# Kernel tuning notes

Measured on AMD Instinct MI355X. Metric: run time of the kernel, lower is better.

Reference implementation:

```python
import jax, jax.numpy as jnp
import numpy as np

B, S, D, H = 2, 2048, 2048, 16
HD = D // H  # head dim = 128

def setup_inputs() -> dict:
    key = jax.random.key(0)
    ks = jax.random.split(key, 5)
    x = jax.random.normal(ks[0], (B, S, D), dtype=jnp.float32)
    # causal mask: True means block that position (per docstring)
    mask = jnp.triu(jnp.ones((S, S), dtype=bool), k=1)
    scale = 1.0 / np.sqrt(D)
    Wq = jax.random.normal(ks[1], (D, D), dtype=jnp.float32) * scale
    Wk = jax.random.normal(ks[2], (D, D), dtype=jnp.float32) * scale
    Wv = jax.random.normal(ks[3], (D, D), dtype=jnp.float32) * scale
    Wo = jax.random.normal(ks[4], (D, D), dtype=jnp.float32) * scale
    return {"x": x, "mask": mask, "Wq": Wq, "Wk": Wk, "Wv": Wv, "Wo": Wo}

def _split_heads(t):
    b, s, _ = t.shape
    return t.reshape(b, s, H, HD).transpose(0, 2, 1, 3)  # (b, h, s, hd)

def reference(x, mask, Wq, Wk, Wv, Wo):
    # nn.Linear(bias=False): y = x @ W.T
    q = _split_heads(x @ Wq.T)
    k = _split_heads(x @ Wk.T)
    v = _split_heads(x @ Wv.T)
    scale = HD ** -0.5
    scores = jnp.einsum('bhqd,bhkd->bhqk', q, k) * scale  # (b,h,s,s)
    scores = jnp.where(mask[None, None, :, :], -jnp.inf, scores)
    weights = jax.nn.softmax(scores, axis=-1)  # dropout is identity at eval
    out = jnp.einsum('bhqk,bhkd->bhqd', weights, v)
    out = out.transpose(0, 2, 1, 3).reshape(x.shape[0], x.shape[1], D)
    return out @ Wo.T
```

## Files before the change

### kernel.cpp

```cpp
#include <hip/hip_runtime.h>
#include <hip/hip_bf16.h>

typedef __bf16 bf16x8 __attribute__((ext_vector_type(8)));
typedef float f32x4 __attribute__((ext_vector_type(4)));
typedef unsigned short ushort8v __attribute__((ext_vector_type(8)));

__device__ __forceinline__ unsigned short f2bf(float f) {
    unsigned int u = __float_as_uint(f);
    u = (u + 0x7fffu + ((u >> 16) & 1u)) >> 16;
    return (unsigned short)u;
}

__device__ __forceinline__ f32x4 mfma16(bf16x8 a, bf16x8 b, f32x4 c) {
    return __builtin_amdgcn_mfma_f32_16x16x32_bf16(a, b, c, 0, 0, 0);
}

__device__ __forceinline__ void store_c(unsigned short* p, float v) { *p = f2bf(v); }
__device__ __forceinline__ void store_c(float* p, float v) { *p = v; }

__global__ __launch_bounds__(256) void cast_f32_bf16(const float* __restrict__ in,
                                                     unsigned short* __restrict__ out,
                                                     int n4) {
    int i = blockIdx.x * blockDim.x + threadIdx.x;
    if (i < n4) {
        float4 f = ((const float4*)in)[i];
        ushort4 u;
        u.x = f2bf(f.x); u.y = f2bf(f.y); u.z = f2bf(f.z); u.w = f2bf(f.w);
        ((ushort4*)out)[i] = u;
    }
}

__global__ __launch_bounds__(256) void transpose_v(const unsigned short* __restrict__ v,
                                                   unsigned short* __restrict__ vt) {
    __shared__ unsigned short t[64][65];
    const int tid = threadIdx.x;
    const int s0 = blockIdx.x * 64;
    const int d0 = blockIdx.y * 64;
    const int bh = blockIdx.z;
    const int b = bh >> 4, h = bh & 15;

#pragma unroll
    for (int i = 0; i < 2; ++i) {
        int idx = i * 256 + tid;
        int r = idx >> 3, c8 = (idx & 7) * 8;
        ushort8v d = *(const ushort8v*)(v + ((size_t)(b * 2048 + s0 + r)) * 2048 + h * 128 + d0 + c8);
#pragma unroll
        for (int j = 0; j < 8; ++j) t[r][c8 + j] = d[j];
    }
    __syncthreads();
#pragma unroll
    for (int i = 0; i < 2; ++i) {
        int idx = i * 256 + tid;
        int dr = idx >> 3, sc8 = (idx & 7) * 8;
        ushort8v o;
#pragma unroll
        for (int j = 0; j < 8; ++j) o[j] = t[sc8 + j][dr];
        *(ushort8v*)(vt + ((size_t)(bh * 128 + d0 + dr)) * 2048 + s0 + sc8) = o;
    }
}

template <typename OUT_T>
__global__ __launch_bounds__(256) void gemm_bt(const unsigned short* __restrict__ A,
                                               const unsigned short* __restrict__ B,
                                               OUT_T* __restrict__ C,
                                               int M, int N, int K) {
    __shared__ __align__(16) unsigned short lA[128 * 64];
    __shared__ __align__(16) unsigned short lB[128 * 64];

    const int tid = threadIdx.x;
    const int w = tid >> 6, lane = tid & 63;
    const int wm = w >> 1, wn = w & 1;
    const int lane16 = lane & 15, g = lane >> 4;
    const int row0 = blockIdx.y * 128, col0 = blockIdx.x * 128;

    f32x4 acc[4][4] = {};

    for (int kt = 0; kt < K; kt += 64) {
#pragma unroll
        for (int i = 0; i < 4; ++i) {
            int ci = (w * 4 + i) * 64 + lane;
            int grow = ci >> 3;
            int gcolb = (ci & 7) * 16;
            size_t aoff = ((size_t)(row0 + grow) * K + kt) * 2 + gcolb;
            size_t boff = ((size_t)(col0 + grow) * K + kt) * 2 + gcolb;
            __builtin_amdgcn_global_load_lds(
                (__attribute__((address_space(1))) void*)(void*)((const char*)A + aoff),
                (__attribute__((address_space(3))) void*)((char*)lA + (w * 4 + i) * 1024),
                16, 0, 0);
            __builtin_amdgcn_global_load_lds(
                (__attribute__((address_space(1))) void*)(void*)((const char*)B + boff),
                (__attribute__((address_space(3))) void*)((char*)lB + (w * 4 + i) * 1024),
                16, 0, 0);
        }
        __syncthreads();
#pragma unroll
        for (int kk = 0; kk < 2; ++kk) {
            bf16x8 aF[4], bF[4];
#pragma unroll
            for (int f = 0; f < 4; ++f) {
                aF[f] = *(const bf16x8*)&lA[(wm * 64 + f * 16 + lane16) * 64 + kk * 32 + g * 8];
                bF[f] = *(const bf16x8*)&lB[(wn * 64 + f * 16 + lane16) * 64 + kk * 32 + g * 8];
            }
#pragma unroll
            for (int fm = 0; fm < 4; ++fm)
#pragma unroll
                for (int fn = 0; fn < 4; ++fn)
                    acc[fm][fn] = mfma16(aF[fm], bF[fn], acc[fm][fn]);
        }
        __syncthreads();
    }

#pragma unroll
    for (int fm = 0; fm < 4; ++fm) {
        int r0 = row0 + wm * 64 + fm * 16 + g * 4;
#pragma unroll
        for (int fn = 0; fn < 4; ++fn) {
            int c = col0 + wn * 64 + fn * 16 + lane16;
#pragma unroll
            for (int r = 0; r < 4; ++r)
                store_c(&C[(size_t)(r0 + r) * N + c], acc[fm][fn][r]);
        }
    }
}

__global__ __launch_bounds__(256) void attn_causal(const unsigned short* __restrict__ Q,
                                                   const unsigned short* __restrict__ K,
                                                   const unsigned short* __restrict__ VT,
                                                   unsigned short* __restrict__ O) {
    __shared__ __align__(16) unsigned short lK[64 * 128];
    __shared__ __align__(16) unsigned short lVt[128 * 64];
    __shared__ __align__(16) unsigned short lP[4][16 * 80];

    const int tid = threadIdx.x, w = tid >> 6, lane = tid & 63;
    const int lane16 = lane & 15, g = lane >> 4;
    const int bh = blockIdx.y;
    const int b = bh >> 4, h = bh & 15;
    const size_t rowBase = (size_t)b * 2048;
    const int hoff = h * 128;
    const float scale = 0.08838834764831845f;

    for (int pass = 0; pass < 2; ++pass) {
        const int qt = pass ? (31 - (int)blockIdx.x) : (int)blockIdx.x;
        const int qt0 = qt * 64;
        const int qr0 = qt0 + w * 16;

        bf16x8 qa[4];
        {
            const unsigned short* qp = Q + (rowBase + qr0 + lane16) * 2048 + hoff;
#pragma unroll
            for (int kk = 0; kk < 4; ++kk)
                qa[kk] = *(const bf16x8*)(qp + kk * 32 + g * 8);
        }

        float m_r[4], l_r[4];
        f32x4 accO[8];
#pragma unroll
        for (int r = 0; r < 4; ++r) { m_r[r] = -1e30f; l_r[r] = 0.f; }
#pragma unroll
        for (int f = 0; f < 8; ++f) accO[f] = f32x4{0.f, 0.f, 0.f, 0.f};

        const int nt = qt + 1;

        for (int t = 0; t < nt; ++t) {
            const int kv0 = t * 64;
            __syncthreads();
#pragma unroll
            for (int i = 0; i < 4; ++i) {
                int ci = (w * 4 + i) * 64 + lane;
                int krow = ci >> 4;
                int kcolb = ((ci & 15) ^ (krow & 7)) * 16;
                size_t goff = ((rowBase + kv0 + krow) * 2048 + hoff) * 2 + kcolb;
                __builtin_amdgcn_global_load_lds(
                    (__attribute__((address_space(1))) void*)(void*)((const char*)K + goff),
                    (__attribute__((address_space(3))) void*)((char*)lK + (w * 4 + i) * 1024),
                    16, 0, 0);
            }
#pragma unroll
            for (int i = 0; i < 4; ++i) {
                int ci = (w * 4 + i) * 64 + lane;
                int drow = ci >> 3;
                int slot = (ci & 7) ^ (drow & 7);
                size_t goff = ((size_t)(bh * 128 + drow) * 2048 + kv0 + slot * 8) * 2;
                __builtin_amdgcn_global_load_lds(
                    (__attribute__((address_space(1))) void*)(void*)((const char*)VT + goff),
                    (__attribute__((address_space(3))) void*)((char*)lVt + (w * 4 + i) * 1024),
                    16, 0, 0);
            }
            __syncthreads();

            float p[4][4];
#pragma unroll
            for (int n = 0; n < 4; ++n) {
                f32x4 sc = {0.f, 0.f, 0.f, 0.f};
                int row = n * 16 + lane16;
#pragma unroll
                for (int kk = 0; kk < 4; ++kk) {
                    int sw = (kk * 4 + g) ^ (row & 7);
                    bf16x8 kb = *(const bf16x8*)&lK[row * 128 + sw * 8];
                    sc = mfma16(qa[kk], kb, sc);
                }
#pragma unroll
                for (int r = 0; r < 4; ++r) p[n][r] = sc[r] * scale;
            }
            if (t == nt - 1) {
#pragma unroll
                for (int n = 0; n < 4; ++n)
#pragma unroll
                    for (int r = 0; r < 4; ++r) {
                        int qi = qr0 + g * 4 + r, ki = kv0 + n * 16 + lane16;
                        if (ki > qi) p[n][r] = -1e30f;
                    }
            }
#pragma unroll
            for (int r = 0; r < 4; ++r) {
                float rm = fmaxf(fmaxf(p[0][r], p[1][r]), fmaxf(p[2][r], p[3][r]));
#pragma unroll
                for (int off = 1; off < 16; off <<= 1)
                    rm = fmaxf(rm, __shfl_xor(rm, off, 64));
                float mn = fmaxf(m_r[r], rm);
                float fac = __expf(m_r[r] - mn);
                float rs = 0.f;
#pragma unroll
                for (int n = 0; n < 4; ++n) { p[n][r] = __expf(p[n][r] - mn); rs += p[n][r]; }
#pragma unroll
                for (int off = 1; off < 16; off <<= 1)
                    rs += __shfl_xor(rs, off, 64);
                l_r[r] = l_r[r] * fac + rs;
                m_r[r] = mn;
#pragma unroll
                for (int f = 0; f < 8; ++f) accO[f][r] *= fac;
            }
#pragma unroll
            for (int n = 0; n < 4; ++n)
#pragma unroll
                for (int r = 0; r < 4; ++r)
                    lP[w][(g * 4 + r) * 80 + n * 16 + lane16] = f2bf(p[n][r]);
            asm volatile("s_waitcnt lgkmcnt(0)" ::: "memory");
#pragma unroll
            for (int kk2 = 0; kk2 < 2; ++kk2) {
                bf16x8 pa = *(const bf16x8*)&lP[w][lane16 * 80 + kk2 * 32 + g * 8];
#pragma unroll
                for (int f = 0; f < 8; ++f) {
                    int row = f * 16 + lane16;
                    int slot = (kk2 * 4 + g) ^ (row & 7);
                    bf16x8 vb = *(const bf16x8*)&lVt[row * 64 + slot * 8];
                    accO[f] = mfma16(pa, vb, accO[f]);
                }
            }
        }

#pragma unroll
        for (int f = 0; f < 8; ++f)
#pragma unroll
            for (int r = 0; r < 4; ++r) {
                float ov = accO[f][r] / l_r[r];
                O[(rowBase + qr0 + g * 4 + r) * 2048 + hoff + f * 16 + lane16] = f2bf(ov);
            }
    }
}

extern "C" void kernel_launch(void* const* d_in, const int* in_sizes, int n_in,
                              void* d_out, int out_size, void* d_ws, size_t ws_size,
                              hipStream_t stream) {
    const float* x  = (const float*)d_in[0];
    const float* Wq = (const float*)d_in[2];
    const float* Wk = (const float*)d_in[3];
    const float* Wv = (const float*)d_in[4];
    const float* Wo = (const float*)d_in[5];
    float* out = (float*)d_out;

    char* ws = (char*)d_ws;
    unsigned short* xb = (unsigned short*)(ws);
    unsigned short* q  = (unsigned short*)(ws + (size_t)(16u << 20));
    unsigned short* k  = (unsigned short*)(ws + (size_t)(32u << 20));
    unsigned short* v  = (unsigned short*)(ws + (size_t)(48u << 20));
    unsigned short* wb = (unsigned short*)(ws + (size_t)(64u << 20));
    unsigned short* vt = xb;
    unsigned short* o  = v;

    const int M = 4096, D = 2048;
    dim3 gg(D / 128, M / 128);

    cast_f32_bf16<<<(M * D / 4) / 256, 256, 0, stream>>>(x, xb, M * D / 4);

    cast_f32_bf16<<<(D * D / 4) / 256, 256, 0, stream>>>(Wq, wb, D * D / 4);
    gemm_bt<unsigned short><<<gg, 256, 0, stream>>>(xb, wb, q, M, D, D);
    cast_f32_bf16<<<(D * D / 4) / 256, 256, 0, stream>>>(Wk, wb, D * D / 4);
    gemm_bt<unsigned short><<<gg, 256, 0, stream>>>(xb, wb, k, M, D, D);
    cast_f32_bf16<<<(D * D / 4) / 256, 256, 0, stream>>>(Wv, wb, D * D / 4);
    gemm_bt<unsigned short><<<gg, 256, 0, stream>>>(xb, wb, v, M, D, D);

    transpose_v<<<dim3(32, 2, 32), 256, 0, stream>>>(v, vt);

    attn_causal<<<dim3(16, 32), 256, 0, stream>>>(q, k, vt, o);

    cast_f32_bf16<<<(D * D / 4) / 256, 256, 0, stream>>>(Wo, wb, D * D / 4);
    gemm_bt<float><<<gg, 256, 0, stream>>>(o, wb, out, M, D, D);
}
```

Before: 461.2 us.

## Rewrite projection GEMM with triple-buffered LDS pipeline, swizzle, and 256x128 tiles

Replaces the single-buffered 128x128 GEMM with a 512-thread kernel that computes 256x128 tiles. It prefetches three K-slices of 32 into rotating LDS buffers, using explicit vmcnt waits so global loads overlap MFMA work. An XOR swizzle is applied to the LDS layout to avoid bank conflicts on fragment reads, and setprio raises wave priority around the MFMA block. The cost is more LDS per block and fewer blocks in the grid, which may reduce occupancy and parallelism across the CUs.

```diff
diff --git a/kernel.cpp b/kernel.cpp
--- a/kernel.cpp
+++ b/kernel.cpp
@@ -59,66 +59,101 @@
     }
 }
 
+__device__ __forceinline__ void stage_tile(const unsigned short* __restrict__ A,
+                                           const unsigned short* __restrict__ B,
+                                           char* lAslot, char* lBslot,
+                                           int row0, int col0, int kt, int K,
+                                           int tid, int w) {
+#pragma unroll
+    for (int j = 0; j < 2; ++j) {
+        int ci = j * 512 + tid;
+        int r = ci >> 2, p = ci & 3;
+        int c = p ^ ((r >> 1) & 3);
+        size_t goff = ((size_t)(row0 + r) * K + kt + c * 8) * 2;
+        __builtin_amdgcn_global_load_lds(
+            (__attribute__((address_space(1))) void*)(void*)((const char*)A + goff),
+            (__attribute__((address_space(3))) void*)(lAslot + (j * 512 + w * 64) * 16),
+            16, 0, 0);
+    }
+    {
+        int ci = tid;
+        int r = ci >> 2, p = ci & 3;
+        int c = p ^ ((r >> 1) & 3);
+        size_t goff = ((size_t)(col0 + r) * K + kt + c * 8) * 2;
+        __builtin_amdgcn_global_load_lds(
+            (__attribute__((address_space(1))) void*)(void*)((const char*)B + goff),
+            (__attribute__((address_space(3))) void*)(lBslot + (w * 64) * 16),
+            16, 0, 0);
+    }
+}
+
 template <typename OUT_T>
-__global__ __launch_bounds__(256) void gemm_bt(const unsigned short* __restrict__ A,
-                                               const unsigned short* __restrict__ B,
-                                               OUT_T* __restrict__ C,
-                                               int M, int N, int K) {
-    __shared__ __align__(16) unsigned short lA[128 * 64];
-    __shared__ __align__(16) unsigned short lB[128 * 64];
+__global__ __launch_bounds__(512) void gemm_bt2(const unsigned short* __restrict__ A,
+                                                const unsigned short* __restrict__ B,
+                                                OUT_T* __restrict__ C,
+                                                int M, int N, int K) {
+    __shared__ __align__(16) unsigned short lA[3][256 * 32];
+    __shared__ __align__(16) unsigned short lB[3][128 * 32];
 
     const int tid = threadIdx.x;
     const int w = tid >> 6, lane = tid & 63;
-    const int wm = w >> 1, wn = w & 1;
+    const int wm = w >> 2, wn = w & 3;
     const int lane16 = lane & 15, g = lane >> 4;
-    const int row0 = blockIdx.y * 128, col0 = blockIdx.x * 128;
-
-    f32x4 acc[4][4] = {};
-
-    for (int kt = 0; kt < K; kt += 64) {
-#pragma unroll
-        for (int i = 0; i < 4; ++i) {
-            int ci = (w * 4 + i) * 64 + lane;
-            int grow = ci >> 3;
-            int gcolb = (ci & 7) * 16;
-            size_t aoff = ((size_t)(row0 + grow) * K + kt) * 2 + gcolb;
-            size_t boff = ((size_t)(col0 + grow) * K + kt) * 2 + gcolb;
-            __builtin_amdgcn_global_load_lds(
-                (__attribute__((address_space(1))) void*)(void*)((const char*)A + aoff),
-                (__attribute__((address_space(3))) void*)((char*)lA + (w * 4 + i) * 1024),
-                16, 0, 0);
-            __builtin_amdgcn_global_load_lds(
-                (__attribute__((address_space(1))) void*)(void*)((const char*)B + boff),
-                (__attribute__((address_space(3))) void*)((char*)lB + (w * 4 + i) * 1024),
-                16, 0, 0);
-        }
-        __syncthreads();
-#pragma unroll
-        for (int kk = 0; kk < 2; ++kk) {
-            bf16x8 aF[4], bF[4];
-#pragma unroll
-            for (int f = 0; f < 4; ++f) {
-                aF[f] = *(const bf16x8*)&lA[(wm * 64 + f * 16 + lane16) * 64 + kk * 32 + g * 8];
-                bF[f] = *(const bf16x8*)&lB[(wn * 64 + f * 16 + lane16) * 64 + kk * 32 + g * 8];
-            }
-#pragma unroll
-            for (int fm = 0; fm < 4; ++fm)
-#pragma unroll
-                for (int fn = 0; fn < 4; ++fn)
-                    acc[fm][fn] = mfma16(aF[fm], bF[fn], acc[fm][fn]);
-        }
-        __syncthreads();
-    }
-
-#pragma unroll
-    for (int fm = 0; fm < 4; ++fm) {
-        int r0 = row0 + wm * 64 + fm * 16 + g * 4;
-#pragma unroll
-        for (int fn = 0; fn < 4; ++fn) {
-            int c = col0 + wn * 64 + fn * 16 + lane16;
+    const int row0 = blockIdx.y * 256, col0 = blockIdx.x * 128;
+    const int NT = K >> 5;
+
+    f32x4 acc[8][2] = {};
+
+    stage_tile(A, B, (char*)lA[0], (char*)lB[0], row0, col0, 0, K, tid, w);
+    stage_tile(A, B, (char*)lA[1], (char*)lB[1], row0, col0, 32, K, tid, w);
+    stage_tile(A, B, (char*)lA[2], (char*)lB[2], row0, col0, 64, K, tid, w);
+
+    int s = 0;
+#pragma unroll 1
+    for (int t = 0; t < NT; ++t) {
+        if (t + 2 < NT)      asm volatile("s_waitcnt vmcnt(6)" ::: "memory");
+        else if (t + 1 < NT) asm volatile("s_waitcnt vmcnt(3)" ::: "memory");
+        else                 asm volatile("s_waitcnt vmcnt(0)" ::: "memory");
+        __builtin_amdgcn_s_barrier();
+        asm volatile("" ::: "memory");
+
+        bf16x8 aF[8], bF[2];
+#pragma unroll
+        for (int mf = 0; mf < 8; ++mf) {
+            int r = wm * 128 + mf * 16 + lane16;
+            aF[mf] = *(const bf16x8*)&lA[s][r * 32 + (g ^ ((r >> 1) & 3)) * 8];
+        }
+#pragma unroll
+        for (int nf = 0; nf < 2; ++nf) {
+            int r = wn * 32 + nf * 16 + lane16;
+            bF[nf] = *(const bf16x8*)&lB[s][r * 32 + (g ^ ((r >> 1) & 3)) * 8];
+        }
+        __builtin_amdgcn_s_setprio(1);
+#pragma unroll
+        for (int mf = 0; mf < 8; ++mf)
+#pragma unroll
+            for (int nf = 0; nf < 2; ++nf)
+                acc[mf][nf] = mfma16(aF[mf], bF[nf], acc[mf][nf]);
+        __builtin_amdgcn_s_setprio(0);
+
+        asm volatile("" ::: "memory");
+        __builtin_amdgcn_s_barrier();
+        asm volatile("" ::: "memory");
+
+        if (t + 3 < NT)
+            stage_tile(A, B, (char*)lA[s], (char*)lB[s], row0, col0, (t + 3) * 32, K, tid, w);
+        s = (s == 2) ? 0 : s + 1;
+    }
+
+#pragma unroll
+    for (int mf = 0; mf < 8; ++mf) {
+        int r0 = row0 + wm * 128 + mf * 16 + g * 4;
+#pragma unroll
+        for (int nf = 0; nf < 2; ++nf) {
+            int c = col0 + wn * 32 + nf * 16 + lane16;
 #pragma unroll
             for (int r = 0; r < 4; ++r)
-                store_c(&C[(size_t)(r0 + r) * N + c], acc[fm][fn][r]);
+                store_c(&C[(size_t)(r0 + r) * N + c], acc[mf][nf][r]);
         }
     }
 }
@@ -279,21 +314,21 @@
     unsigned short* o  = v;
 
     const int M = 4096, D = 2048;
-    dim3 gg(D / 128, M / 128);
+    dim3 gg(D / 128, M / 256);
 
     cast_f32_bf16<<<(M * D / 4) / 256, 256, 0, stream>>>(x, xb, M * D / 4);
 
     cast_f32_bf16<<<(D * D / 4) / 256, 256, 0, stream>>>(Wq, wb, D * D / 4);
-    gemm_bt<unsigned short><<<gg, 256, 0, stream>>>(xb, wb, q, M, D, D);
+    gemm_bt2<unsigned short><<<gg, 512, 0, stream>>>(xb, wb, q, M, D, D);
     cast_f32_bf16<<<(D * D / 4) / 256, 256, 0, stream>>>(Wk, wb, D * D / 4);
-    gemm_bt<unsigned short><<<gg, 256, 0, stream>>>(xb, wb, k, M, D, D);
+    gemm_bt2<unsigned short><<<gg, 512, 0, stream>>>(xb, wb, k, M, D, D);
     cast_f32_bf16<<<(D * D / 4) / 256, 256, 0, stream>>>(Wv, wb, D * D / 4);
-    gemm_bt<unsigned short><<<gg, 256, 0, stream>>>(xb, wb, v, M, D, D);
+    gemm_bt2<unsigned short><<<gg, 512, 0, stream>>>(xb, wb, v, M, D, D);
 
     transpose_v<<<dim3(32, 2, 32), 256, 0, stream>>>(v, vt);
 
     attn_causal<<<dim3(16, 32), 256, 0, stream>>>(q, k, vt, o);
 
     cast_f32_bf16<<<(D * D / 4) / 256, 256, 0, stream>>>(Wo, wb, D * D / 4);
-    gemm_bt<float><<<gg, 256, 0, stream>>>(o, wb, out, M, D, D);
-}
+    gemm_bt2<float><<<gg, 512, 0, stream>>>(o, wb, out, M, D, D);
+}
```

After: 487.8 us. 5.8% more time.
